# Optimization experiments

Measured on AMD Instinct MI355X. Metric: run time of the kernel, lower is better.

Reference implementation:

```python
import jax, jax.numpy as jnp
import numpy as np

B, T, D = 2, 2048, 1024
HEADS, UNITS = 16, 64
OUT_DIM = 1024
_LARGE_BIAS = 10000.0


def _uniform(key, shape, fan_in, fan_out):
    limit = np.sqrt(6.0 / (fan_in + fan_out))
    return jax.random.uniform(key, shape, jnp.float32, -limit, limit)


def setup_inputs() -> dict:
    key = jax.random.key(0)
    kx, kq, kk, kv, ko = jax.random.split(key, 5)
    x = jax.random.normal(kx, (B, T, D), jnp.float32)
    mask = jnp.ones((B, T), jnp.int32)
    Wq = _uniform(kq, (D, HEADS * UNITS), D, UNITS)
    Wk = _uniform(kk, (D, HEADS * UNITS), D, UNITS)
    Wv = _uniform(kv, (D, HEADS * UNITS), D, UNITS)
    Wo = _uniform(ko, (HEADS * UNITS, OUT_DIM), HEADS * UNITS, OUT_DIM)
    return {"x": x, "mask": mask, "Wq": Wq, "Wk": Wk, "Wv": Wv, "Wo": Wo}


def reference(x, mask, Wq, Wk, Wv, Wo):
    m = mask.astype(x.dtype)                      # [B, T]
    x = x * m[:, :, None]                         # zero padded positions
    b, t, _ = x.shape
    # projections, split heads: [B, T, H, U]
    q = (x @ Wq).reshape(b, t, HEADS, UNITS)
    k = (x @ Wk).reshape(b, t, HEADS, UNITS)
    v = (x @ Wv).reshape(b, t, HEADS, UNITS)
    # logits[b,h,i,j] = sum_u q[b,i,h,u] k[b,j,h,u]
    logits = jnp.einsum('bihu,bjhu->bhij', q, k) / np.sqrt(UNITS).astype(x.dtype)
    # causal (forward) mask: subtract large bias above the diagonal
    causal = jnp.triu(jnp.full((t, t), _LARGE_BIAS, x.dtype), k=1)
    logits = logits - causal
    # padding mask on key axis
    logits = logits - ((1.0 - m) * _LARGE_BIAS)[:, None, None, :]
    weights = jax.nn.softmax(logits, axis=-1)     # [B, H, T, T]
    attended = jnp.einsum('bhij,bjhu->bihu', weights, v)
    attended = attended.reshape(b, t, HEADS * UNITS)
    return attended @ Wo                          # [B, T, OUT_DIM]
```

## Files before the change

kernel.cpp:

```cpp
#include <hip/hip_runtime.h>
#include <stdint.h>
#include <stddef.h>

#define B_ 2
#define T_ 2048
#define D_ 1024
#define H_ 16
#define U_ 64
#define M_ (B_ * T_)
#define N_ (H_ * U_)

typedef __attribute__((ext_vector_type(4))) float f32x4;
typedef __attribute__((ext_vector_type(8))) short s16x8;
typedef __attribute__((ext_vector_type(8))) __bf16 b16x8;

static_assert(sizeof(s16x8) == 16, "frag size");

__device__ __forceinline__ unsigned short f2bf(float f) {
  unsigned int u = __float_as_uint(f);
  u += 0x7FFFu + ((u >> 16) & 1u);
  return (unsigned short)(u >> 16);
}

template <typename V>
__device__ __forceinline__ auto mfma16_impl(V a, V b, f32x4 c, int)
    -> decltype(__builtin_amdgcn_mfma_f32_16x16x32_bf16(a, b, c, 0, 0, 0)) {
  return __builtin_amdgcn_mfma_f32_16x16x32_bf16(a, b, c, 0, 0, 0);
}
template <typename V>
__device__ __forceinline__ f32x4 mfma16_impl(V a, V b, f32x4 c, long) {
  return __builtin_amdgcn_mfma_f32_16x16x32_bf16(
      __builtin_bit_cast(b16x8, a), __builtin_bit_cast(b16x8, b), c, 0, 0, 0);
}
__device__ __forceinline__ f32x4 mfma16(s16x8 a, s16x8 b, f32x4 c) {
  return mfma16_impl(a, b, c, 0);
}

__device__ __forceinline__ void gld16(const unsigned short* g, unsigned short* l) {
  __builtin_amdgcn_global_load_lds(
      (const __attribute__((address_space(1))) void*)g,
      (__attribute__((address_space(3))) void*)l, 16, 0, 0);
}

__global__ void wtrans_kernel(const float* __restrict__ w0, const float* __restrict__ w1,
                              const float* __restrict__ w2, const float* __restrict__ w3,
                              unsigned short* __restrict__ o0, unsigned short* __restrict__ o1,
                              unsigned short* __restrict__ o2, unsigned short* __restrict__ o3) {
  __shared__ float tile[64][65];
  const float* w;
  unsigned short* o;
  switch (blockIdx.z) {
    case 0: w = w0; o = o0; break;
    case 1: w = w1; o = o1; break;
    case 2: w = w2; o = o2; break;
    default: w = w3; o = o3; break;
  }
  const int kb = blockIdx.y * 64, nb = blockIdx.x * 64;
  const int tid = threadIdx.x;
  const int r0 = tid >> 6, c = tid & 63;
#pragma unroll
  for (int i = 0; i < 16; i++) {
    int r = i * 4 + r0;
    tile[r][c] = w[(size_t)(kb + r) * 1024 + nb + c];
  }
  __syncthreads();
#pragma unroll
  for (int i = 0; i < 16; i++) {
    int r = i * 4 + r0;
    o[(size_t)(nb + r) * 1024 + kb + c] = f2bf(tile[c][r]);
  }
}

__global__ void xmask_kernel(const float* __restrict__ x, const int* __restrict__ mask,
                             unsigned short* __restrict__ xb) {
  const int idx = (blockIdx.x * 256 + threadIdx.x) * 4;
  const int row = idx >> 10;
  const float m = (float)mask[row];
  float4 v = *(const float4*)(x + idx);
  ushort4 o;
  o.x = f2bf(v.x * m);
  o.y = f2bf(v.y * m);
  o.z = f2bf(v.z * m);
  o.w = f2bf(v.w * m);
  *(ushort4*)(xb + idx) = o;
}

template <bool OUTF32>
__device__ __forceinline__ void gemm97_body(const unsigned short* __restrict__ A,
                                            const unsigned short* __restrict__ Bt,
                                            void* __restrict__ Cout) {
  constexpr int Kd = 1024, Nd = 1024;
  __shared__ unsigned short la[128 * 32];
  __shared__ unsigned short lb[128 * 32];
  const int tid = threadIdx.x;
  const int lane = tid & 63;
  const int w = tid >> 6;
  const int mb = blockIdx.y * 128, nb = blockIdx.x * 128;
  const int wm = (w >> 1) * 64, wn = (w & 1) * 64;
  const int lr = lane & 15, lg = lane >> 4;
  const int srow = w * 16 + (lane >> 2);
  const int scol = (lane & 3) * 8;
  const unsigned short* gA = A + (size_t)(mb + srow) * Kd + scol;
  const unsigned short* gB = Bt + (size_t)(nb + srow) * Kd + scol;
  unsigned short* lA = la + srow * 32 + scol;
  unsigned short* lB = lb + srow * 32 + scol;

  f32x4 acc[4][4] = {};

  for (int kt = 0; kt < Kd; kt += 32) {
    gld16(gA + kt, lA);
    gld16(gA + kt + (size_t)64 * Kd, lA + 64 * 32);
    gld16(gB + kt, lB);
    gld16(gB + kt + (size_t)64 * Kd, lB + 64 * 32);
    __syncthreads();
    s16x8 af[4], bfr[4];
#pragma unroll
    for (int i = 0; i < 4; i++)
      af[i] = *(const s16x8*)(la + (wm + i * 16 + lr) * 32 + lg * 8);
#pragma unroll
    for (int j = 0; j < 4; j++)
      bfr[j] = *(const s16x8*)(lb + (wn + j * 16 + lr) * 32 + lg * 8);
#pragma unroll
    for (int i = 0; i < 4; i++)
#pragma unroll
      for (int j = 0; j < 4; j++)
        acc[i][j] = mfma16(af[i], bfr[j], acc[i][j]);
    __syncthreads();
  }

#pragma unroll
  for (int i = 0; i < 4; i++)
#pragma unroll
    for (int j = 0; j < 4; j++) {
      const int col = nb + wn + j * 16 + lr;
      const int rowb = mb + wm + i * 16 + lg * 4;
      if (OUTF32) {
        float* C = (float*)Cout;
#pragma unroll
        for (int r = 0; r < 4; r++) C[(size_t)(rowb + r) * Nd + col] = acc[i][j][r];
      } else {
        unsigned short* C = (unsigned short*)Cout;
#pragma unroll
        for (int r = 0; r < 4; r++) C[(size_t)(rowb + r) * Nd + col] = f2bf(acc[i][j][r]);
      }
    }
}

__global__ __launch_bounds__(256) void gemm_qkv(const unsigned short* __restrict__ A,
                                                const unsigned short* __restrict__ wq,
                                                const unsigned short* __restrict__ wk,
                                                const unsigned short* __restrict__ wv,
                                                unsigned short* __restrict__ cq,
                                                unsigned short* __restrict__ ck,
                                                unsigned short* __restrict__ cv) {
  const unsigned short* Bt;
  unsigned short* C;
  if (blockIdx.z == 0) { Bt = wq; C = cq; }
  else if (blockIdx.z == 1) { Bt = wk; C = ck; }
  else { Bt = wv; C = cv; }
  gemm97_body<false>(A, Bt, C);
}

__global__ __launch_bounds__(256) void gemm_out(const unsigned short* __restrict__ A,
                                                const unsigned short* __restrict__ woT,
                                                float* __restrict__ C) {
  gemm97_body<true>(A, woT, C);
}

__global__ void vtrans_kernel(const unsigned short* __restrict__ vb,
                              unsigned short* __restrict__ vt) {
  __shared__ unsigned short tile[64][65];
  const int bh = blockIdx.y;
  const int tb = blockIdx.x * 64;
  const int tid = threadIdx.x;
  const int r0 = tid >> 6, c = tid & 63;
  const unsigned short* src = vb + ((size_t)(bh >> 4) * T_ + tb) * 1024 + (bh & 15) * 64;
#pragma unroll
  for (int i = 0; i < 16; i++) {
    int r = i * 4 + r0;
    tile[r][c] = src[(size_t)r * 1024 + c];
  }
  __syncthreads();
  unsigned short* dst = vt + (size_t)bh * 64 * T_ + tb;
#pragma unroll
  for (int i = 0; i < 16; i++) {
    int u = i * 4 + r0;
    dst[(size_t)u * T_ + c] = tile[c][u];
  }
}

__global__ __launch_bounds__(64, 2) void attn5_kernel(const unsigned short* __restrict__ Q,
                                                      const unsigned short* __restrict__ K,
                                                      const unsigned short* __restrict__ Vt,
                                                      const int* __restrict__ mask,
                                                      unsigned short* __restrict__ att) {
  __shared__ unsigned short pbuf[32 * 64];
  const int lane = threadIdx.x & 63;
  const int li = lane & 15, lg = lane >> 4;
  const int bh = blockIdx.x;
  const int b = bh >> 4, h = bh & 15;
  const int qg = 63 - blockIdx.y;
  const int q0 = qg * 32;

  const float CS = 0.125f * 1.44269504089f;
  const float PB = 10000.0f * 1.44269504089f;

  s16x8 qf[2][2];
#pragma unroll
  for (int f = 0; f < 2; f++) {
    const unsigned short* qrow = Q + ((size_t)(b * T_) + q0 + f * 16 + li) * 1024 + h * 64;
    qf[f][0] = *(const s16x8*)(qrow + lg * 8);
    qf[f][1] = *(const s16x8*)(qrow + 32 + lg * 8);
  }

  const unsigned short* Kb = K + (size_t)(b * T_) * 1024 + h * 64;
  const unsigned short* Vtb = Vt + (size_t)bh * 64 * T_;
  const int* mk = mask + b * T_;

  const int iq0 = q0 + li, iq1 = q0 + 16 + li;

  float mrun[2] = {-1e30f, -1e30f}, lrun[2] = {0.f, 0.f};
  f32x4 acc[4][2] = {};

  const int xr = (li & 3) << 5;
  char* pbb = (char*)pbuf;

  const int ntiles = (q0 + 95) >> 6;
  for (int t = 0; t < ntiles; t++) {
    const int jb = t * 64;
    const bool diag = (jb + 64 > q0);

    f32x4 s[4][2] = {};
#pragma unroll
    for (int jf = 0; jf < 4; jf++) {
      const unsigned short* kr = Kb + (size_t)(jb + jf * 16 + li) * 1024 + lg * 8;
      s16x8 ka = *(const s16x8*)kr;
      s16x8 kc = *(const s16x8*)(kr + 32);
      s[jf][0] = mfma16(ka, qf[0][0], s[jf][0]);
      s[jf][0] = mfma16(kc, qf[0][1], s[jf][0]);
      s[jf][1] = mfma16(ka, qf[1][0], s[jf][1]);
      s[jf][1] = mfma16(kc, qf[1][1], s[jf][1]);
    }

    s16x8 vf[4][2];
#pragma unroll
    for (int uf = 0; uf < 4; uf++) {
      const unsigned short* vr = Vtb + (size_t)(uf * 16 + li) * T_ + jb + lg * 8;
      vf[uf][0] = *(const s16x8*)vr;
      vf[uf][1] = *(const s16x8*)(vr + 32);
    }

    float bias[4][4];
#pragma unroll
    for (int jf = 0; jf < 4; jf++) {
      int4 mv = *(const int4*)(mk + jb + jf * 16 + lg * 4);
      bias[jf][0] = mv.x ? 0.f : -PB;
      bias[jf][1] = mv.y ? 0.f : -PB;
      bias[jf][2] = mv.z ? 0.f : -PB;
      bias[jf][3] = mv.w ? 0.f : -PB;
    }

#pragma unroll
    for (int f = 0; f < 2; f++) {
      const int iq = f ? iq1 : iq0;
      float pmax = -1e30f;
#pragma unroll
      for (int jf = 0; jf < 4; jf++) {
        f32x4 zz;
#pragma unroll
        for (int r = 0; r < 4; r++) {
          float z = fmaf(s[jf][f][r], CS, bias[jf][r]);
          if (diag && (jb + jf * 16 + lg * 4 + r > iq)) z = -1e30f;
          zz[r] = z;
          pmax = fmaxf(pmax, z);
        }
        s[jf][f] = zz;
      }
      pmax = fmaxf(pmax, __shfl_xor(pmax, 16));
      pmax = fmaxf(pmax, __shfl_xor(pmax, 32));
      if (!__all(pmax <= mrun[f])) {
        const float mnew = fmaxf(mrun[f], pmax);
        const float al = exp2f(mrun[f] - mnew);
        lrun[f] *= al;
#pragma unroll
        for (int uf = 0; uf < 4; uf++) acc[uf][f] *= al;
        mrun[f] = mnew;
      }
      const float mm = mrun[f];
      float psum = 0.f;
#pragma unroll
      for (int jf = 0; jf < 4; jf++) {
        ushort4 w4;
#pragma unroll
        for (int r = 0; r < 4; r++) {
          const float p = exp2f(s[jf][f][r] - mm);
          psum += p;
          ((unsigned short*)&w4)[r] = __builtin_bit_cast(unsigned short, (__bf16)p);
        }
        const int wb = (((f * 16 + li) * 64 + jf * 16 + lg * 4) * 2) ^ xr;
        *(ushort4*)(pbb + wb) = w4;
      }
      psum += __shfl_xor(psum, 16);
      psum += __shfl_xor(psum, 32);
      lrun[f] += psum;
    }

    s16x8 pfrag[2][2];
#pragma unroll
    for (int f = 0; f < 2; f++)
#pragma unroll
      for (int hh = 0; hh < 2; hh++) {
        const int rd = (((f * 16 + li) * 64 + hh * 32 + lg * 8) * 2) ^ xr;
        pfrag[f][hh] = *(const s16x8*)(pbb + rd);
      }
#pragma unroll
    for (int uf = 0; uf < 4; uf++)
#pragma unroll
      for (int f = 0; f < 2; f++) {
        acc[uf][f] = mfma16(vf[uf][0], pfrag[f][0], acc[uf][f]);
        acc[uf][f] = mfma16(vf[uf][1], pfrag[f][1], acc[uf][f]);
      }
  }

#pragma unroll
  for (int f = 0; f < 2; f++) {
    const float inv = 1.0f / lrun[f];
    unsigned short* arow = att + ((size_t)(b * T_) + q0 + f * 16 + li) * 1024 + h * 64;
#pragma unroll
    for (int uf = 0; uf < 4; uf++) {
      ushort4 o;
#pragma unroll
      for (int r = 0; r < 4; r++)
        ((unsigned short*)&o)[r] = __builtin_bit_cast(unsigned short, (__bf16)(acc[uf][f][r] * inv));
      *(ushort4*)(arow + uf * 16 + lg * 4) = o;
    }
  }
}

extern "C" void kernel_launch(void* const* d_in, const int* in_sizes, int n_in,
                              void* d_out, int out_size, void* d_ws, size_t ws_size,
                              hipStream_t stream) {
  const float* x = (const float*)d_in[0];
  const int* mask = (const int*)d_in[1];
  const float* Wq = (const float*)d_in[2];
  const float* Wk = (const float*)d_in[3];
  const float* Wv = (const float*)d_in[4];
  const float* Wo = (const float*)d_in[5];

  const size_t MB = 1u << 20;
  char* ws = (char*)d_ws;
  unsigned short* wqT = (unsigned short*)(ws + 0 * MB);
  unsigned short* wkT = (unsigned short*)(ws + 2 * MB);
  unsigned short* wvT = (unsigned short*)(ws + 4 * MB);
  unsigned short* woT = (unsigned short*)(ws + 6 * MB);
  unsigned short* xb  = (unsigned short*)(ws + 8 * MB);
  unsigned short* qb  = (unsigned short*)(ws + 16 * MB);
  unsigned short* kb  = (unsigned short*)(ws + 24 * MB);
  unsigned short* vb  = (unsigned short*)(ws + 32 * MB);
  unsigned short* vt  = xb;
  unsigned short* att = vb;
  (void)ws_size; (void)in_sizes; (void)n_in; (void)out_size;

  wtrans_kernel<<<dim3(16, 16, 4), 256, 0, stream>>>(Wq, Wk, Wv, Wo, wqT, wkT, wvT, woT);
  xmask_kernel<<<dim3(4096), 256, 0, stream>>>(x, mask, xb);
  gemm_qkv<<<dim3(8, 32, 3), 256, 0, stream>>>(xb, wqT, wkT, wvT, qb, kb, vb);
  vtrans_kernel<<<dim3(32, 32), 256, 0, stream>>>(vb, vt);
  attn5_kernel<<<dim3(32, 64), 64, 0, stream>>>(qb, kb, vt, mask, att);
  gemm_out<<<dim3(8, 32), 256, 0, stream>>>(att, woT, (float*)d_out);
}
```

Baseline: 161.3 us.

## Fuse V transpose into QKV GEMM epilogue and halve attention query tile

The QKV GEMM now writes V directly in transposed [b,h,u,t] layout from its epilogue, which removes the separate vtrans kernel and its extra read and write of V. The attention kernel processes 16 query rows per wavefront instead of 32, doubling the grid and raising the occupancy hint to 4 waves per SIMD. The aim is better load balance and latency hiding across the causal triangle. In exchange, each K/V tile is loaded by twice as many wavefronts, which adds global and cache traffic.

```diff
diff --git a/kernel.cpp b/kernel.cpp
--- a/kernel.cpp
+++ b/kernel.cpp
@@ -85,7 +85,7 @@
   *(ushort4*)(xb + idx) = o;
 }
 
-template <bool OUTF32>
+template <int MODE>
 __device__ __forceinline__ void gemm97_body(const unsigned short* __restrict__ A,
                                             const unsigned short* __restrict__ Bt,
                                             void* __restrict__ Cout) {
@@ -134,14 +134,21 @@
     for (int j = 0; j < 4; j++) {
       const int col = nb + wn + j * 16 + lr;
       const int rowb = mb + wm + i * 16 + lg * 4;
-      if (OUTF32) {
+      if (MODE == 1) {
         float* C = (float*)Cout;
 #pragma unroll
         for (int r = 0; r < 4; r++) C[(size_t)(rowb + r) * Nd + col] = acc[i][j][r];
+      } else if (MODE == 0) {
+        unsigned short* C = (unsigned short*)Cout;
+#pragma unroll
+        for (int r = 0; r < 4; r++) C[(size_t)(rowb + r) * Nd + col] = f2bf(acc[i][j][r]);
       } else {
         unsigned short* C = (unsigned short*)Cout;
-#pragma unroll
-        for (int r = 0; r < 4; r++) C[(size_t)(rowb + r) * Nd + col] = f2bf(acc[i][j][r]);
+        const size_t vrow = ((size_t)(rowb >> 11) * 16 + (col >> 6)) * 64 + (col & 63);
+        ushort4 o;
+#pragma unroll
+        for (int r = 0; r < 4; r++) ((unsigned short*)&o)[r] = f2bf(acc[i][j][r]);
+        *(ushort4*)(C + vrow * T_ + (rowb & 2047)) = o;
       }
     }
 }
@@ -152,94 +159,67 @@
                                                 const unsigned short* __restrict__ wv,
                                                 unsigned short* __restrict__ cq,
                                                 unsigned short* __restrict__ ck,
-                                                unsigned short* __restrict__ cv) {
-  const unsigned short* Bt;
-  unsigned short* C;
-  if (blockIdx.z == 0) { Bt = wq; C = cq; }
-  else if (blockIdx.z == 1) { Bt = wk; C = ck; }
-  else { Bt = wv; C = cv; }
-  gemm97_body<false>(A, Bt, C);
+                                                unsigned short* __restrict__ vt) {
+  if (blockIdx.z == 0) {
+    gemm97_body<0>(A, wq, cq);
+  } else if (blockIdx.z == 1) {
+    gemm97_body<0>(A, wk, ck);
+  } else {
+    gemm97_body<2>(A, wv, vt);
+  }
 }
 
 __global__ __launch_bounds__(256) void gemm_out(const unsigned short* __restrict__ A,
                                                 const unsigned short* __restrict__ woT,
                                                 float* __restrict__ C) {
-  gemm97_body<true>(A, woT, C);
-}
-
-__global__ void vtrans_kernel(const unsigned short* __restrict__ vb,
-                              unsigned short* __restrict__ vt) {
-  __shared__ unsigned short tile[64][65];
-  const int bh = blockIdx.y;
-  const int tb = blockIdx.x * 64;
-  const int tid = threadIdx.x;
-  const int r0 = tid >> 6, c = tid & 63;
-  const unsigned short* src = vb + ((size_t)(bh >> 4) * T_ + tb) * 1024 + (bh & 15) * 64;
-#pragma unroll
-  for (int i = 0; i < 16; i++) {
-    int r = i * 4 + r0;
-    tile[r][c] = src[(size_t)r * 1024 + c];
-  }
-  __syncthreads();
-  unsigned short* dst = vt + (size_t)bh * 64 * T_ + tb;
-#pragma unroll
-  for (int i = 0; i < 16; i++) {
-    int u = i * 4 + r0;
-    dst[(size_t)u * T_ + c] = tile[c][u];
-  }
-}
-
-__global__ __launch_bounds__(64, 2) void attn5_kernel(const unsigned short* __restrict__ Q,
+  gemm97_body<1>(A, woT, C);
+}
+
+__global__ __launch_bounds__(64, 4) void attn6_kernel(const unsigned short* __restrict__ Q,
                                                       const unsigned short* __restrict__ K,
                                                       const unsigned short* __restrict__ Vt,
                                                       const int* __restrict__ mask,
                                                       unsigned short* __restrict__ att) {
-  __shared__ unsigned short pbuf[32 * 64];
+  __shared__ unsigned short pbuf[16 * 64];
   const int lane = threadIdx.x & 63;
   const int li = lane & 15, lg = lane >> 4;
   const int bh = blockIdx.x;
   const int b = bh >> 4, h = bh & 15;
-  const int qg = 63 - blockIdx.y;
-  const int q0 = qg * 32;
+  const int qg = 127 - blockIdx.y;
+  const int q0 = qg * 16;
 
   const float CS = 0.125f * 1.44269504089f;
   const float PB = 10000.0f * 1.44269504089f;
 
-  s16x8 qf[2][2];
-#pragma unroll
-  for (int f = 0; f < 2; f++) {
-    const unsigned short* qrow = Q + ((size_t)(b * T_) + q0 + f * 16 + li) * 1024 + h * 64;
-    qf[f][0] = *(const s16x8*)(qrow + lg * 8);
-    qf[f][1] = *(const s16x8*)(qrow + 32 + lg * 8);
-  }
+  const unsigned short* qrow = Q + ((size_t)(b * T_) + q0 + li) * 1024 + h * 64;
+  s16x8 qf0 = *(const s16x8*)(qrow + lg * 8);
+  s16x8 qf1 = *(const s16x8*)(qrow + 32 + lg * 8);
 
   const unsigned short* Kb = K + (size_t)(b * T_) * 1024 + h * 64;
   const unsigned short* Vtb = Vt + (size_t)bh * 64 * T_;
   const int* mk = mask + b * T_;
 
-  const int iq0 = q0 + li, iq1 = q0 + 16 + li;
-
-  float mrun[2] = {-1e30f, -1e30f}, lrun[2] = {0.f, 0.f};
-  f32x4 acc[4][2] = {};
+  const int iq = q0 + li;
+
+  float mrun = -1e30f, lrun = 0.f;
+  f32x4 acc[4] = {};
 
   const int xr = (li & 3) << 5;
   char* pbb = (char*)pbuf;
 
-  const int ntiles = (q0 + 95) >> 6;
+  const int ntiles = (q0 + 79) >> 6;
   for (int t = 0; t < ntiles; t++) {
     const int jb = t * 64;
     const bool diag = (jb + 64 > q0);
 
-    f32x4 s[4][2] = {};
+    f32x4 s[4] = {};
 #pragma unroll
     for (int jf = 0; jf < 4; jf++) {
       const unsigned short* kr = Kb + (size_t)(jb + jf * 16 + li) * 1024 + lg * 8;
       s16x8 ka = *(const s16x8*)kr;
       s16x8 kc = *(const s16x8*)(kr + 32);
-      s[jf][0] = mfma16(ka, qf[0][0], s[jf][0]);
-      s[jf][0] = mfma16(kc, qf[0][1], s[jf][0]);
-      s[jf][1] = mfma16(ka, qf[1][0], s[jf][1]);
-      s[jf][1] = mfma16(kc, qf[1][1], s[jf][1]);
+      s[jf] = mfma16(ka, qf0, s[jf]);
+      s[jf] = mfma16(kc, qf1, s[jf]);
     }
 
     s16x8 vf[4][2];
@@ -260,80 +240,68 @@
       bias[jf][3] = mv.w ? 0.f : -PB;
     }
 
-#pragma unroll
-    for (int f = 0; f < 2; f++) {
-      const int iq = f ? iq1 : iq0;
-      float pmax = -1e30f;
-#pragma unroll
-      for (int jf = 0; jf < 4; jf++) {
-        f32x4 zz;
-#pragma unroll
-        for (int r = 0; r < 4; r++) {
-          float z = fmaf(s[jf][f][r], CS, bias[jf][r]);
-          if (diag && (jb + jf * 16 + lg * 4 + r > iq)) z = -1e30f;
-          zz[r] = z;
-          pmax = fmaxf(pmax, z);
-        }
-        s[jf][f] = zz;
+    float pmax = -1e30f;
+#pragma unroll
+    for (int jf = 0; jf < 4; jf++) {
+      f32x4 zz;
+#pragma unroll
+      for (int r = 0; r < 4; r++) {
+        float z = fmaf(s[jf][r], CS, bias[jf][r]);
+        if (diag && (jb + jf * 16 + lg * 4 + r > iq)) z = -1e30f;
+        zz[r] = z;
+        pmax = fmaxf(pmax, z);
       }
-      pmax = fmaxf(pmax, __shfl_xor(pmax, 16));
-      pmax = fmaxf(pmax, __shfl_xor(pmax, 32));
-      if (!__all(pmax <= mrun[f])) {
-        const float mnew = fmaxf(mrun[f], pmax);
-        const float al = exp2f(mrun[f] - mnew);
-        lrun[f] *= al;
-#pragma unroll
-        for (int uf = 0; uf < 4; uf++) acc[uf][f] *= al;
-        mrun[f] = mnew;
+      s[jf] = zz;
+    }
+    pmax = fmaxf(pmax, __shfl_xor(pmax, 16));
+    pmax = fmaxf(pmax, __shfl_xor(pmax, 32));
+    if (!__all(pmax <= mrun)) {
+      const float mnew = fmaxf(mrun, pmax);
+      const float al = exp2f(mrun - mnew);
+      lrun *= al;
+#pragma unroll
+      for (int uf = 0; uf < 4; uf++) acc[uf] *= al;
+      mrun = mnew;
+    }
+    float psum = 0.f;
+#pragma unroll
+    for (int jf = 0; jf < 4; jf++) {
+      ushort4 w4;
+#pragma unroll
+      for (int r = 0; r < 4; r++) {
+        const float p = exp2f(s[jf][r] - mrun);
+        psum += p;
+        ((unsigned short*)&w4)[r] = __builtin_bit_cast(unsigned short, (__bf16)p);
       }
-      const float mm = mrun[f];
-      float psum = 0.f;
-#pragma unroll
-      for (int jf = 0; jf < 4; jf++) {
-        ushort4 w4;
-#pragma unroll
-        for (int r = 0; r < 4; r++) {
-          const float p = exp2f(s[jf][f][r] - mm);
-          psum += p;
-          ((unsigned short*)&w4)[r] = __builtin_bit_cast(unsigned short, (__bf16)p);
-        }
-        const int wb = (((f * 16 + li) * 64 + jf * 16 + lg * 4) * 2) ^ xr;
-        *(ushort4*)(pbb + wb) = w4;
-      }
-      psum += __shfl_xor(psum, 16);
-      psum += __shfl_xor(psum, 32);
-      lrun[f] += psum;
-    }
-
-    s16x8 pfrag[2][2];
-#pragma unroll
-    for (int f = 0; f < 2; f++)
-#pragma unroll
-      for (int hh = 0; hh < 2; hh++) {
-        const int rd = (((f * 16 + li) * 64 + hh * 32 + lg * 8) * 2) ^ xr;
-        pfrag[f][hh] = *(const s16x8*)(pbb + rd);
-      }
-#pragma unroll
-    for (int uf = 0; uf < 4; uf++)
-#pragma unroll
-      for (int f = 0; f < 2; f++) {
-        acc[uf][f] = mfma16(vf[uf][0], pfrag[f][0], acc[uf][f]);
-        acc[uf][f] = mfma16(vf[uf][1], pfrag[f][1], acc[uf][f]);
-      }
-  }
-
-#pragma unroll
-  for (int f = 0; f < 2; f++) {
-    const float inv = 1.0f / lrun[f];
-    unsigned short* arow = att + ((size_t)(b * T_) + q0 + f * 16 + li) * 1024 + h * 64;
+      const int wb = ((li * 64 + jf * 16 + lg * 4) * 2) ^ xr;
+      *(ushort4*)(pbb + wb) = w4;
+    }
+    psum += __shfl_xor(psum, 16);
+    psum += __shfl_xor(psum, 32);
+    lrun += psum;
+
+    s16x8 pfrag[2];
+#pragma unroll
+    for (int hh = 0; hh < 2; hh++) {
+      const int rd = ((li * 64 + hh * 32 + lg * 8) * 2) ^ xr;
+      pfrag[hh] = *(const s16x8*)(pbb + rd);
+    }
 #pragma unroll
     for (int uf = 0; uf < 4; uf++) {
-      ushort4 o;
-#pragma unroll
-      for (int r = 0; r < 4; r++)
-        ((unsigned short*)&o)[r] = __builtin_bit_cast(unsigned short, (__bf16)(acc[uf][f][r] * inv));
-      *(ushort4*)(arow + uf * 16 + lg * 4) = o;
-    }
+      acc[uf] = mfma16(vf[uf][0], pfrag[0], acc[uf]);
+      acc[uf] = mfma16(vf[uf][1], pfrag[1], acc[uf]);
+    }
+  }
+
+  const float inv = 1.0f / lrun;
+  unsigned short* arow = att + ((size_t)(b * T_) + q0 + li) * 1024 + h * 64;
+#pragma unroll
+  for (int uf = 0; uf < 4; uf++) {
+    ushort4 o;
+#pragma unroll
+    for (int r = 0; r < 4; r++)
+      ((unsigned short*)&o)[r] = __builtin_bit_cast(unsigned short, (__bf16)(acc[uf][r] * inv));
+    *(ushort4*)(arow + uf * 16 + lg * 4) = o;
   }
 }
 
@@ -356,15 +324,13 @@
   unsigned short* xb  = (unsigned short*)(ws + 8 * MB);
   unsigned short* qb  = (unsigned short*)(ws + 16 * MB);
   unsigned short* kb  = (unsigned short*)(ws + 24 * MB);
-  unsigned short* vb  = (unsigned short*)(ws + 32 * MB);
-  unsigned short* vt  = xb;
-  unsigned short* att = vb;
+  unsigned short* vt  = (unsigned short*)(ws + 32 * MB);
+  unsigned short* att = xb;
   (void)ws_size; (void)in_sizes; (void)n_in; (void)out_size;
 
   wtrans_kernel<<<dim3(16, 16, 4), 256, 0, stream>>>(Wq, Wk, Wv, Wo, wqT, wkT, wvT, woT);
   xmask_kernel<<<dim3(4096), 256, 0, stream>>>(x, mask, xb);
-  gemm_qkv<<<dim3(8, 32, 3), 256, 0, stream>>>(xb, wqT, wkT, wvT, qb, kb, vb);
-  vtrans_kernel<<<dim3(32, 32), 256, 0, stream>>>(vb, vt);
-  attn5_kernel<<<dim3(32, 64), 64, 0, stream>>>(qb, kb, vt, mask, att);
+  gemm_qkv<<<dim3(8, 32, 3), 256, 0, stream>>>(xb, wqT, wkT, wvT, qb, kb, vt);
+  attn6_kernel<<<dim3(32, 128), 64, 0, stream>>>(qb, kb, vt, mask, att);
   gemm_out<<<dim3(8, 32), 256, 0, stream>>>(att, woT, (float*)d_out);
 }
```

Result: slower. 206.1 us (+27.8%).

## Fuse V transpose into QKV GEMM epilogue and share K/V tiles via LDS

Applied to the files above, without the earlier changes.

The V projection GEMM now writes its output directly in transposed per-head layout, which removes the separate vtrans kernel and its round trip through memory. The attention kernel moves from one-wave blocks to four-wave blocks that cover 128 query rows. The waves share double-buffered K and V tiles staged in swizzled LDS through async global-to-LDS loads, so each K/V tile is read from global memory once per block instead of once per wave. The cost is block-wide barriers on every tile, idle waves on the causal-diagonal tiles, and more LDS per block, which may limit occupancy.

```diff
diff --git a/kernel.cpp b/kernel.cpp
--- a/kernel.cpp
+++ b/kernel.cpp
@@ -85,7 +85,7 @@
   *(ushort4*)(xb + idx) = o;
 }
 
-template <bool OUTF32>
+template <int MODE>
 __device__ __forceinline__ void gemm97_body(const unsigned short* __restrict__ A,
                                             const unsigned short* __restrict__ Bt,
                                             void* __restrict__ Cout) {
@@ -134,14 +134,21 @@
     for (int j = 0; j < 4; j++) {
       const int col = nb + wn + j * 16 + lr;
       const int rowb = mb + wm + i * 16 + lg * 4;
-      if (OUTF32) {
+      if (MODE == 1) {
         float* C = (float*)Cout;
 #pragma unroll
         for (int r = 0; r < 4; r++) C[(size_t)(rowb + r) * Nd + col] = acc[i][j][r];
+      } else if (MODE == 0) {
+        unsigned short* C = (unsigned short*)Cout;
+#pragma unroll
+        for (int r = 0; r < 4; r++) C[(size_t)(rowb + r) * Nd + col] = f2bf(acc[i][j][r]);
       } else {
         unsigned short* C = (unsigned short*)Cout;
-#pragma unroll
-        for (int r = 0; r < 4; r++) C[(size_t)(rowb + r) * Nd + col] = f2bf(acc[i][j][r]);
+        const size_t vrow = ((size_t)(rowb >> 11) * 16 + (col >> 6)) * 64 + (col & 63);
+        ushort4 o;
+#pragma unroll
+        for (int r = 0; r < 4; r++) ((unsigned short*)&o)[r] = f2bf(acc[i][j][r]);
+        *(ushort4*)(C + vrow * T_ + (rowb & 2047)) = o;
       }
     }
 }
@@ -152,58 +159,45 @@
                                                 const unsigned short* __restrict__ wv,
                                                 unsigned short* __restrict__ cq,
                                                 unsigned short* __restrict__ ck,
-                                                unsigned short* __restrict__ cv) {
-  const unsigned short* Bt;
-  unsigned short* C;
-  if (blockIdx.z == 0) { Bt = wq; C = cq; }
-  else if (blockIdx.z == 1) { Bt = wk; C = ck; }
-  else { Bt = wv; C = cv; }
-  gemm97_body<false>(A, Bt, C);
+                                                unsigned short* __restrict__ vt) {
+  if (blockIdx.z == 0) {
+    gemm97_body<0>(A, wq, cq);
+  } else if (blockIdx.z == 1) {
+    gemm97_body<0>(A, wk, ck);
+  } else {
+    gemm97_body<2>(A, wv, vt);
+  }
 }
 
 __global__ __launch_bounds__(256) void gemm_out(const unsigned short* __restrict__ A,
                                                 const unsigned short* __restrict__ woT,
                                                 float* __restrict__ C) {
-  gemm97_body<true>(A, woT, C);
-}
-
-__global__ void vtrans_kernel(const unsigned short* __restrict__ vb,
-                              unsigned short* __restrict__ vt) {
-  __shared__ unsigned short tile[64][65];
-  const int bh = blockIdx.y;
-  const int tb = blockIdx.x * 64;
+  gemm97_body<1>(A, woT, C);
+}
+
+__global__ __launch_bounds__(256, 2) void attn7_kernel(const unsigned short* __restrict__ Q,
+                                                       const unsigned short* __restrict__ K,
+                                                       const unsigned short* __restrict__ Vt,
+                                                       const int* __restrict__ mask,
+                                                       unsigned short* __restrict__ att) {
+  __shared__ unsigned short kls[2][64 * 64];
+  __shared__ unsigned short vls[2][64 * 64];
+  __shared__ unsigned short pbuf[4][32 * 64];
   const int tid = threadIdx.x;
-  const int r0 = tid >> 6, c = tid & 63;
-  const unsigned short* src = vb + ((size_t)(bh >> 4) * T_ + tb) * 1024 + (bh & 15) * 64;
-#pragma unroll
-  for (int i = 0; i < 16; i++) {
-    int r = i * 4 + r0;
-    tile[r][c] = src[(size_t)r * 1024 + c];
-  }
-  __syncthreads();
-  unsigned short* dst = vt + (size_t)bh * 64 * T_ + tb;
-#pragma unroll
-  for (int i = 0; i < 16; i++) {
-    int u = i * 4 + r0;
-    dst[(size_t)u * T_ + c] = tile[c][u];
-  }
-}
-
-__global__ __launch_bounds__(64, 2) void attn5_kernel(const unsigned short* __restrict__ Q,
-                                                      const unsigned short* __restrict__ K,
-                                                      const unsigned short* __restrict__ Vt,
-                                                      const int* __restrict__ mask,
-                                                      unsigned short* __restrict__ att) {
-  __shared__ unsigned short pbuf[32 * 64];
-  const int lane = threadIdx.x & 63;
+  const int w = tid >> 6, lane = tid & 63;
   const int li = lane & 15, lg = lane >> 4;
   const int bh = blockIdx.x;
   const int b = bh >> 4, h = bh & 15;
-  const int qg = 63 - blockIdx.y;
-  const int q0 = qg * 32;
+  const int qb = 15 - blockIdx.y;
+  const int q0 = qb * 128 + w * 32;
+  const int ntiles = qb * 2 + 2;
 
   const float CS = 0.125f * 1.44269504089f;
   const float PB = 10000.0f * 1.44269504089f;
+
+  const unsigned short* Kb = K + (size_t)(b * T_) * 1024 + h * 64;
+  const unsigned short* Vtb = Vt + (size_t)bh * 64 * T_;
+  const int* mk = mask + b * T_;
 
   s16x8 qf[2][2];
 #pragma unroll
@@ -213,113 +207,133 @@
     qf[f][1] = *(const s16x8*)(qrow + 32 + lg * 8);
   }
 
-  const unsigned short* Kb = K + (size_t)(b * T_) * 1024 + h * 64;
-  const unsigned short* Vtb = Vt + (size_t)bh * 64 * T_;
-  const int* mk = mask + b * T_;
-
-  const int iq0 = q0 + li, iq1 = q0 + 16 + li;
+  const int srow = tid >> 3;
+  const int scol = (tid & 7) * 8;
+  const int sc0 = scol ^ ((srow & 7) << 3);
+  const unsigned short* kg0 = Kb + (size_t)srow * 1024 + sc0;
+  const unsigned short* kg1 = Kb + (size_t)(srow + 32) * 1024 + sc0;
+  const unsigned short* vg0 = Vtb + (size_t)srow * T_ + sc0;
+  const unsigned short* vg1 = Vtb + (size_t)(srow + 32) * T_ + sc0;
+  const int dst0 = srow * 64 + scol, dst1 = (srow + 32) * 64 + scol;
 
   float mrun[2] = {-1e30f, -1e30f}, lrun[2] = {0.f, 0.f};
   f32x4 acc[4][2] = {};
 
+  const int iq0 = q0 + li, iq1 = q0 + 16 + li;
+  const int kswz = (li & 7) << 3;
   const int xr = (li & 3) << 5;
-  char* pbb = (char*)pbuf;
-
-  const int ntiles = (q0 + 95) >> 6;
+  char* pbb = (char*)&pbuf[w][0];
+
+  gld16(kg0, &kls[0][dst0]);
+  gld16(kg1, &kls[0][dst1]);
+  gld16(vg0, &vls[0][dst0]);
+  gld16(vg1, &vls[0][dst1]);
+  __syncthreads();
+
   for (int t = 0; t < ntiles; t++) {
     const int jb = t * 64;
-    const bool diag = (jb + 64 > q0);
-
-    f32x4 s[4][2] = {};
-#pragma unroll
-    for (int jf = 0; jf < 4; jf++) {
-      const unsigned short* kr = Kb + (size_t)(jb + jf * 16 + li) * 1024 + lg * 8;
-      s16x8 ka = *(const s16x8*)kr;
-      s16x8 kc = *(const s16x8*)(kr + 32);
-      s[jf][0] = mfma16(ka, qf[0][0], s[jf][0]);
-      s[jf][0] = mfma16(kc, qf[0][1], s[jf][0]);
-      s[jf][1] = mfma16(ka, qf[1][0], s[jf][1]);
-      s[jf][1] = mfma16(kc, qf[1][1], s[jf][1]);
+    const int cur = t & 1;
+    if (t + 1 < ntiles) {
+      const size_t go = (size_t)(t + 1) * 64 * 1024;
+      gld16(kg0 + go, &kls[cur ^ 1][dst0]);
+      gld16(kg1 + go, &kls[cur ^ 1][dst1]);
+      gld16(vg0 + (t + 1) * 64, &vls[cur ^ 1][dst0]);
+      gld16(vg1 + (t + 1) * 64, &vls[cur ^ 1][dst1]);
     }
 
-    s16x8 vf[4][2];
-#pragma unroll
-    for (int uf = 0; uf < 4; uf++) {
-      const unsigned short* vr = Vtb + (size_t)(uf * 16 + li) * T_ + jb + lg * 8;
-      vf[uf][0] = *(const s16x8*)vr;
-      vf[uf][1] = *(const s16x8*)(vr + 32);
+    if (jb <= q0 + 31) {
+      const bool diag = (jb + 64 > q0);
+      const unsigned short* kt_ = &kls[cur][0];
+      const unsigned short* vt_ = &vls[cur][0];
+
+      f32x4 s[4][2] = {};
+#pragma unroll
+      for (int jf = 0; jf < 4; jf++) {
+        const int krow = (jf * 16 + li) * 64;
+        s16x8 ka = *(const s16x8*)(kt_ + krow + ((lg * 8) ^ kswz));
+        s16x8 kc = *(const s16x8*)(kt_ + krow + ((32 + lg * 8) ^ kswz));
+        s[jf][0] = mfma16(ka, qf[0][0], s[jf][0]);
+        s[jf][0] = mfma16(kc, qf[0][1], s[jf][0]);
+        s[jf][1] = mfma16(ka, qf[1][0], s[jf][1]);
+        s[jf][1] = mfma16(kc, qf[1][1], s[jf][1]);
+      }
+
+      float bias[4][4];
+#pragma unroll
+      for (int jf = 0; jf < 4; jf++) {
+        int4 mv = *(const int4*)(mk + jb + jf * 16 + lg * 4);
+        bias[jf][0] = mv.x ? 0.f : -PB;
+        bias[jf][1] = mv.y ? 0.f : -PB;
+        bias[jf][2] = mv.z ? 0.f : -PB;
+        bias[jf][3] = mv.w ? 0.f : -PB;
+      }
+
+#pragma unroll
+      for (int f = 0; f < 2; f++) {
+        const int iq = f ? iq1 : iq0;
+        float pmax = -1e30f;
+#pragma unroll
+        for (int jf = 0; jf < 4; jf++) {
+          f32x4 zz;
+#pragma unroll
+          for (int r = 0; r < 4; r++) {
+            float z = fmaf(s[jf][f][r], CS, bias[jf][r]);
+            if (diag && (jb + jf * 16 + lg * 4 + r > iq)) z = -1e30f;
+            zz[r] = z;
+            pmax = fmaxf(pmax, z);
+          }
+          s[jf][f] = zz;
+        }
+        pmax = fmaxf(pmax, __shfl_xor(pmax, 16));
+        pmax = fmaxf(pmax, __shfl_xor(pmax, 32));
+        if (!__all(pmax <= mrun[f])) {
+          const float mnew = fmaxf(mrun[f], pmax);
+          const float al = exp2f(mrun[f] - mnew);
+          lrun[f] *= al;
+#pragma unroll
+          for (int uf = 0; uf < 4; uf++) acc[uf][f] *= al;
+          mrun[f] = mnew;
+        }
+        const float mm = mrun[f];
+        float psum = 0.f;
+#pragma unroll
+        for (int jf = 0; jf < 4; jf++) {
+          ushort4 w4;
+#pragma unroll
+          for (int r = 0; r < 4; r++) {
+            const float p = exp2f(s[jf][f][r] - mm);
+            psum += p;
+            ((unsigned short*)&w4)[r] = __builtin_bit_cast(unsigned short, (__bf16)p);
+          }
+          const int wb = (((f * 16 + li) * 64 + jf * 16 + lg * 4) * 2) ^ xr;
+          *(ushort4*)(pbb + wb) = w4;
+        }
+        psum += __shfl_xor(psum, 16);
+        psum += __shfl_xor(psum, 32);
+        lrun[f] += psum;
+      }
+
+      s16x8 pfrag[2][2];
+#pragma unroll
+      for (int f = 0; f < 2; f++)
+#pragma unroll
+        for (int hh = 0; hh < 2; hh++) {
+          const int rd = (((f * 16 + li) * 64 + hh * 32 + lg * 8) * 2) ^ xr;
+          pfrag[f][hh] = *(const s16x8*)(pbb + rd);
+        }
+#pragma unroll
+      for (int uf = 0; uf < 4; uf++) {
+        const int vrow = (uf * 16 + li) * 64;
+        s16x8 v0 = *(const s16x8*)(vt_ + vrow + ((lg * 8) ^ kswz));
+        s16x8 v1 = *(const s16x8*)(vt_ + vrow + ((32 + lg * 8) ^ kswz));
+#pragma unroll
+        for (int f = 0; f < 2; f++) {
+          acc[uf][f] = mfma16(v0, pfrag[f][0], acc[uf][f]);
+          acc[uf][f] = mfma16(v1, pfrag[f][1], acc[uf][f]);
+        }
+      }
     }
-
-    float bias[4][4];
-#pragma unroll
-    for (int jf = 0; jf < 4; jf++) {
-      int4 mv = *(const int4*)(mk + jb + jf * 16 + lg * 4);
-      bias[jf][0] = mv.x ? 0.f : -PB;
-      bias[jf][1] = mv.y ? 0.f : -PB;
-      bias[jf][2] = mv.z ? 0.f : -PB;
-      bias[jf][3] = mv.w ? 0.f : -PB;
-    }
-
-#pragma unroll
-    for (int f = 0; f < 2; f++) {
-      const int iq = f ? iq1 : iq0;
-      float pmax = -1e30f;
-#pragma unroll
-      for (int jf = 0; jf < 4; jf++) {
-        f32x4 zz;
-#pragma unroll
-        for (int r = 0; r < 4; r++) {
-          float z = fmaf(s[jf][f][r], CS, bias[jf][r]);
-          if (diag && (jb + jf * 16 + lg * 4 + r > iq)) z = -1e30f;
-          zz[r] = z;
-          pmax = fmaxf(pmax, z);
-        }
-        s[jf][f] = zz;
-      }
-      pmax = fmaxf(pmax, __shfl_xor(pmax, 16));
-      pmax = fmaxf(pmax, __shfl_xor(pmax, 32));
-      if (!__all(pmax <= mrun[f])) {
-        const float mnew = fmaxf(mrun[f], pmax);
-        const float al = exp2f(mrun[f] - mnew);
-        lrun[f] *= al;
-#pragma unroll
-        for (int uf = 0; uf < 4; uf++) acc[uf][f] *= al;
-        mrun[f] = mnew;
-      }
-      const float mm = mrun[f];
-      float psum = 0.f;
-#pragma unroll
-      for (int jf = 0; jf < 4; jf++) {
-        ushort4 w4;
-#pragma unroll
-        for (int r = 0; r < 4; r++) {
-          const float p = exp2f(s[jf][f][r] - mm);
-          psum += p;
-          ((unsigned short*)&w4)[r] = __builtin_bit_cast(unsigned short, (__bf16)p);
-        }
-        const int wb = (((f * 16 + li) * 64 + jf * 16 + lg * 4) * 2) ^ xr;
-        *(ushort4*)(pbb + wb) = w4;
-      }
-      psum += __shfl_xor(psum, 16);
-      psum += __shfl_xor(psum, 32);
-      lrun[f] += psum;
-    }
-
-    s16x8 pfrag[2][2];
-#pragma unroll
-    for (int f = 0; f < 2; f++)
-#pragma unroll
-      for (int hh = 0; hh < 2; hh++) {
-        const int rd = (((f * 16 + li) * 64 + hh * 32 + lg * 8) * 2) ^ xr;
-        pfrag[f][hh] = *(const s16x8*)(pbb + rd);
-      }
-#pragma unroll
-    for (int uf = 0; uf < 4; uf++)
-#pragma unroll
-      for (int f = 0; f < 2; f++) {
-        acc[uf][f] = mfma16(vf[uf][0], pfrag[f][0], acc[uf][f]);
-        acc[uf][f] = mfma16(vf[uf][1], pfrag[f][1], acc[uf][f]);
-      }
+    __syncthreads();
   }
 
 #pragma unroll
@@ -356,15 +370,13 @@
   unsigned short* xb  = (unsigned short*)(ws + 8 * MB);
   unsigned short* qb  = (unsigned short*)(ws + 16 * MB);
   unsigned short* kb  = (unsigned short*)(ws + 24 * MB);
-  unsigned short* vb  = (unsigned short*)(ws + 32 * MB);
-  unsigned short* vt  = xb;
-  unsigned short* att = vb;
+  unsigned short* vt  = (unsigned short*)(ws + 32 * MB);
+  unsigned short* att = xb;
   (void)ws_size; (void)in_sizes; (void)n_in; (void)out_size;
 
   wtrans_kernel<<<dim3(16, 16, 4), 256, 0, stream>>>(Wq, Wk, Wv, Wo, wqT, wkT, wvT, woT);
   xmask_kernel<<<dim3(4096), 256, 0, stream>>>(x, mask, xb);
-  gemm_qkv<<<dim3(8, 32, 3), 256, 0, stream>>>(xb, wqT, wkT, wvT, qb, kb, vb);
-  vtrans_kernel<<<dim3(32, 32), 256, 0, stream>>>(vb, vt);
-  attn5_kernel<<<dim3(32, 64), 64, 0, stream>>>(qb, kb, vt, mask, att);
+  gemm_qkv<<<dim3(8, 32, 3), 256, 0, stream>>>(xb, wqT, wkT, wvT, qb, kb, vt);
+  attn7_kernel<<<dim3(32, 16), 256, 0, stream>>>(qb, kb, vt, mask, att);
   gemm_out<<<dim3(8, 32), 256, 0, stream>>>(att, woT, (float*)d_out);
 }
```

Result: slower. 171.0 us (+6.1%).

## Fuse V transpose into QKV GEMM and split attention KV tiles across two waves

Applied to the files above, without the earlier changes.

The V projection GEMM now writes its output directly in the transposed per-head layout, which removes the separate vtrans kernel and its extra read and write of V. The attention kernel uses two waves per block. Each wave handles alternate key tiles, and the two partial softmax states are merged through shared memory at the end. s_setprio is placed around the MFMA sections to favour the matrix work. This adds parallelism for the long causal rows at the cost of a merge step, more LDS and a block-level barrier.

```diff
diff --git a/kernel.cpp b/kernel.cpp
--- a/kernel.cpp
+++ b/kernel.cpp
@@ -85,7 +85,7 @@
   *(ushort4*)(xb + idx) = o;
 }
 
-template <bool OUTF32>
+template <int MODE>
 __device__ __forceinline__ void gemm97_body(const unsigned short* __restrict__ A,
                                             const unsigned short* __restrict__ Bt,
                                             void* __restrict__ Cout) {
@@ -134,14 +134,21 @@
     for (int j = 0; j < 4; j++) {
       const int col = nb + wn + j * 16 + lr;
       const int rowb = mb + wm + i * 16 + lg * 4;
-      if (OUTF32) {
+      if (MODE == 1) {
         float* C = (float*)Cout;
 #pragma unroll
         for (int r = 0; r < 4; r++) C[(size_t)(rowb + r) * Nd + col] = acc[i][j][r];
+      } else if (MODE == 0) {
+        unsigned short* C = (unsigned short*)Cout;
+#pragma unroll
+        for (int r = 0; r < 4; r++) C[(size_t)(rowb + r) * Nd + col] = f2bf(acc[i][j][r]);
       } else {
         unsigned short* C = (unsigned short*)Cout;
-#pragma unroll
-        for (int r = 0; r < 4; r++) C[(size_t)(rowb + r) * Nd + col] = f2bf(acc[i][j][r]);
+        const size_t vrow = ((size_t)(rowb >> 11) * 16 + (col >> 6)) * 64 + (col & 63);
+        ushort4 o;
+#pragma unroll
+        for (int r = 0; r < 4; r++) ((unsigned short*)&o)[r] = f2bf(acc[i][j][r]);
+        *(ushort4*)(C + vrow * T_ + (rowb & 2047)) = o;
       }
     }
 }
@@ -152,50 +159,31 @@
                                                 const unsigned short* __restrict__ wv,
                                                 unsigned short* __restrict__ cq,
                                                 unsigned short* __restrict__ ck,
-                                                unsigned short* __restrict__ cv) {
-  const unsigned short* Bt;
-  unsigned short* C;
-  if (blockIdx.z == 0) { Bt = wq; C = cq; }
-  else if (blockIdx.z == 1) { Bt = wk; C = ck; }
-  else { Bt = wv; C = cv; }
-  gemm97_body<false>(A, Bt, C);
+                                                unsigned short* __restrict__ vt) {
+  if (blockIdx.z == 0) {
+    gemm97_body<0>(A, wq, cq);
+  } else if (blockIdx.z == 1) {
+    gemm97_body<0>(A, wk, ck);
+  } else {
+    gemm97_body<2>(A, wv, vt);
+  }
 }
 
 __global__ __launch_bounds__(256) void gemm_out(const unsigned short* __restrict__ A,
                                                 const unsigned short* __restrict__ woT,
                                                 float* __restrict__ C) {
-  gemm97_body<true>(A, woT, C);
-}
-
-__global__ void vtrans_kernel(const unsigned short* __restrict__ vb,
-                              unsigned short* __restrict__ vt) {
-  __shared__ unsigned short tile[64][65];
-  const int bh = blockIdx.y;
-  const int tb = blockIdx.x * 64;
+  gemm97_body<1>(A, woT, C);
+}
+
+__global__ __launch_bounds__(128, 4) void attn8_kernel(const unsigned short* __restrict__ Q,
+                                                       const unsigned short* __restrict__ K,
+                                                       const unsigned short* __restrict__ Vt,
+                                                       const int* __restrict__ mask,
+                                                       unsigned short* __restrict__ att) {
+  __shared__ unsigned short pbuf[2][32 * 64];
+  __shared__ float cb[36 * 64];
   const int tid = threadIdx.x;
-  const int r0 = tid >> 6, c = tid & 63;
-  const unsigned short* src = vb + ((size_t)(bh >> 4) * T_ + tb) * 1024 + (bh & 15) * 64;
-#pragma unroll
-  for (int i = 0; i < 16; i++) {
-    int r = i * 4 + r0;
-    tile[r][c] = src[(size_t)r * 1024 + c];
-  }
-  __syncthreads();
-  unsigned short* dst = vt + (size_t)bh * 64 * T_ + tb;
-#pragma unroll
-  for (int i = 0; i < 16; i++) {
-    int u = i * 4 + r0;
-    dst[(size_t)u * T_ + c] = tile[c][u];
-  }
-}
-
-__global__ __launch_bounds__(64, 2) void attn5_kernel(const unsigned short* __restrict__ Q,
-                                                      const unsigned short* __restrict__ K,
-                                                      const unsigned short* __restrict__ Vt,
-                                                      const int* __restrict__ mask,
-                                                      unsigned short* __restrict__ att) {
-  __shared__ unsigned short pbuf[32 * 64];
-  const int lane = threadIdx.x & 63;
+  const int w = tid >> 6, lane = tid & 63;
   const int li = lane & 15, lg = lane >> 4;
   const int bh = blockIdx.x;
   const int b = bh >> 4, h = bh & 15;
@@ -223,14 +211,15 @@
   f32x4 acc[4][2] = {};
 
   const int xr = (li & 3) << 5;
-  char* pbb = (char*)pbuf;
+  char* pbb = (char*)&pbuf[w][0];
 
   const int ntiles = (q0 + 95) >> 6;
-  for (int t = 0; t < ntiles; t++) {
+  for (int t = w; t < ntiles; t += 2) {
     const int jb = t * 64;
     const bool diag = (jb + 64 > q0);
 
     f32x4 s[4][2] = {};
+    __builtin_amdgcn_s_setprio(1);
 #pragma unroll
     for (int jf = 0; jf < 4; jf++) {
       const unsigned short* kr = Kb + (size_t)(jb + jf * 16 + li) * 1024 + lg * 8;
@@ -241,6 +230,7 @@
       s[jf][1] = mfma16(ka, qf[1][0], s[jf][1]);
       s[jf][1] = mfma16(kc, qf[1][1], s[jf][1]);
     }
+    __builtin_amdgcn_s_setprio(0);
 
     s16x8 vf[4][2];
 #pragma unroll
@@ -313,6 +303,7 @@
         const int rd = (((f * 16 + li) * 64 + hh * 32 + lg * 8) * 2) ^ xr;
         pfrag[f][hh] = *(const s16x8*)(pbb + rd);
       }
+    __builtin_amdgcn_s_setprio(1);
 #pragma unroll
     for (int uf = 0; uf < 4; uf++)
 #pragma unroll
@@ -320,19 +311,44 @@
         acc[uf][f] = mfma16(vf[uf][0], pfrag[f][0], acc[uf][f]);
         acc[uf][f] = mfma16(vf[uf][1], pfrag[f][1], acc[uf][f]);
       }
-  }
-
-#pragma unroll
-  for (int f = 0; f < 2; f++) {
-    const float inv = 1.0f / lrun[f];
-    unsigned short* arow = att + ((size_t)(b * T_) + q0 + f * 16 + li) * 1024 + h * 64;
-#pragma unroll
-    for (int uf = 0; uf < 4; uf++) {
-      ushort4 o;
-#pragma unroll
-      for (int r = 0; r < 4; r++)
-        ((unsigned short*)&o)[r] = __builtin_bit_cast(unsigned short, (__bf16)(acc[uf][f][r] * inv));
-      *(ushort4*)(arow + uf * 16 + lg * 4) = o;
+    __builtin_amdgcn_s_setprio(0);
+  }
+
+  if (w == 1) {
+#pragma unroll
+    for (int f = 0; f < 2; f++)
+#pragma unroll
+      for (int uf = 0; uf < 4; uf++)
+#pragma unroll
+        for (int r = 0; r < 4; r++)
+          cb[(f * 16 + uf * 4 + r) * 64 + lane] = acc[uf][f][r];
+    cb[32 * 64 + lane] = mrun[0];
+    cb[33 * 64 + lane] = mrun[1];
+    cb[34 * 64 + lane] = lrun[0];
+    cb[35 * 64 + lane] = lrun[1];
+  }
+  __syncthreads();
+  if (w == 0) {
+#pragma unroll
+    for (int f = 0; f < 2; f++) {
+      const float mB = cb[(32 + f) * 64 + lane];
+      const float lB = cb[(34 + f) * 64 + lane];
+      const float m = fmaxf(mrun[f], mB);
+      const float aA = exp2f(mrun[f] - m);
+      const float aB = exp2f(mB - m);
+      const float inv = 1.0f / (aA * lrun[f] + aB * lB);
+      unsigned short* arow = att + ((size_t)(b * T_) + q0 + f * 16 + li) * 1024 + h * 64;
+#pragma unroll
+      for (int uf = 0; uf < 4; uf++) {
+        ushort4 o;
+#pragma unroll
+        for (int r = 0; r < 4; r++) {
+          const float vB = cb[(f * 16 + uf * 4 + r) * 64 + lane];
+          const float v = (aA * acc[uf][f][r] + aB * vB) * inv;
+          ((unsigned short*)&o)[r] = __builtin_bit_cast(unsigned short, (__bf16)v);
+        }
+        *(ushort4*)(arow + uf * 16 + lg * 4) = o;
+      }
     }
   }
 }
@@ -356,15 +372,13 @@
   unsigned short* xb  = (unsigned short*)(ws + 8 * MB);
   unsigned short* qb  = (unsigned short*)(ws + 16 * MB);
   unsigned short* kb  = (unsigned short*)(ws + 24 * MB);
-  unsigned short* vb  = (unsigned short*)(ws + 32 * MB);
-  unsigned short* vt  = xb;
-  unsigned short* att = vb;
+  unsigned short* vt  = (unsigned short*)(ws + 32 * MB);
+  unsigned short* att = xb;
   (void)ws_size; (void)in_sizes; (void)n_in; (void)out_size;
 
   wtrans_kernel<<<dim3(16, 16, 4), 256, 0, stream>>>(Wq, Wk, Wv, Wo, wqT, wkT, wvT, woT);
   xmask_kernel<<<dim3(4096), 256, 0, stream>>>(x, mask, xb);
-  gemm_qkv<<<dim3(8, 32, 3), 256, 0, stream>>>(xb, wqT, wkT, wvT, qb, kb, vb);
-  vtrans_kernel<<<dim3(32, 32), 256, 0, stream>>>(vb, vt);
-  attn5_kernel<<<dim3(32, 64), 64, 0, stream>>>(qb, kb, vt, mask, att);
+  gemm_qkv<<<dim3(8, 32, 3), 256, 0, stream>>>(xb, wqT, wkT, wvT, qb, kb, vt);
+  attn8_kernel<<<dim3(32, 64), 128, 0, stream>>>(qb, kb, vt, mask, att);
   gemm_out<<<dim3(8, 32), 256, 0, stream>>>(att, woT, (float*)d_out);
 }
```

Result: slower. 263.2 us (+63.2%).
